# Kernel tuning notes

Measured on AMD Instinct MI355X. Metric: run time of the kernel, lower is better.

The kernel has to match this reference:

```python
import jax, jax.numpy as jnp
import numpy as np

C, H, W = 64, 32, 32
N = 32
HW = H * W
EPS = 1e-5


def setup_inputs() -> dict:
    kk = jax.random.key(0)
    ks = jax.random.split(kk, 6)
    shp = (N, C, H, W)
    return {
        "query": jax.random.normal(ks[0], shp, jnp.float32),
        "key": jax.random.normal(ks[1], shp, jnp.float32),
        "value": jax.random.normal(ks[2], shp, jnp.float32),
        "ln1_w": jnp.ones((C, H, W), jnp.float32),
        "ln1_b": jnp.zeros((C, H, W), jnp.float32),
        "ln2_w": jnp.ones((C, H, W), jnp.float32),
        "ln2_b": jnp.zeros((C, H, W), jnp.float32),
        "ln3_w": jnp.ones((C, H, W), jnp.float32),
        "ln3_b": jnp.zeros((C, H, W), jnp.float32),
        "wq": jax.random.normal(ks[3], (C, C), jnp.float32) / np.sqrt(C).astype(np.float32),
        "bq": jnp.zeros((C,), jnp.float32),
        "wk": jax.random.normal(ks[4], (C, C), jnp.float32) / np.sqrt(C).astype(np.float32),
        "bk": jnp.zeros((C,), jnp.float32),
        "wv": jax.random.normal(ks[5], (C, C), jnp.float32) / np.sqrt(C).astype(np.float32),
        "bv": jnp.zeros((C,), jnp.float32),
    }


def _ln(x, w, b):
    # LayerNorm over the full (C,H,W) normalized_shape, as nn.LayerNorm(dim)
    mu = jnp.mean(x, axis=(1, 2, 3), keepdims=True)
    var = jnp.var(x, axis=(1, 2, 3), keepdims=True)
    return (x - mu) * jax.lax.rsqrt(var + EPS) * w + b


def _proj(x, w, b):
    # 1x1 conv == per-pixel channel mixing; output reshaped to (N, C, H*W)
    y = jnp.einsum('oc,nchw->nohw', w, x) + b[None, :, None, None]
    return y.reshape(x.shape[0], C, HW)


def reference(query, key, value, ln1_w, ln1_b, ln2_w, ln2_b, ln3_w, ln3_b,
              wq, bq, wk, bk, wv, bv):
    qn = _ln(query, ln1_w, ln1_b)
    kn = _ln(key, ln2_w, ln2_b)
    vn = _ln(value, ln3_w, ln3_b)
    q = _proj(qn, wq, bq)   # (N, C, HW)
    k = _proj(kn, wk, bk)
    v = _proj(vn, wv, bv)
    # attention[n,i,j] = sum_c k[n,c,i] * q[n,c,j] / sqrt(C); softmax over dim=1 (i)
    attn = jnp.einsum('nci,ncj->nij', k, q) / jnp.sqrt(jnp.float32(C))
    attn = jax.nn.softmax(attn, axis=1)
    # output = v @ attn : (N, C, HW)
    out = jnp.einsum('nci,nij->ncj', v, attn).reshape(qn.shape)
    # residual adds the NORMALIZED query (that's what SelfAttention receives)
    x = (qn + out).reshape(qn.shape[0], -1)  # (N, C*H*W)
    return x, attn
```

## Files before the change

kernel.cpp:

```cpp
#include <hip/hip_runtime.h>
#include <math.h>

#define NB   32
#define CCH  64
#define HWD  1024
#define CHW  65536
#define EPSV 1e-5f

typedef __attribute__((ext_vector_type(8))) short bf16x8;
typedef __attribute__((ext_vector_type(4))) float f32x4;

__device__ __forceinline__ unsigned f2b(float x) {
    union { float f; unsigned u; } v; v.f = x;
    return (v.u + 0x7fffu + ((v.u >> 16) & 1u)) >> 16;
}
__device__ __forceinline__ float b2f(unsigned short u) {
    union { unsigned u; float f; } v; v.u = ((unsigned)u) << 16;
    return v.f;
}

__global__ __launch_bounds__(256)
void k_stats(const float* __restrict__ q, const float* __restrict__ k,
             const float* __restrict__ v, float* __restrict__ part)
{
    const int chunk = blockIdx.x, which = blockIdx.y, n = blockIdx.z;
    const float* x = (which == 0) ? q : (which == 1 ? k : v);
    const float4* x4 = (const float4*)(x + (size_t)n * CHW) + chunk * 2048;
    float s = 0.f, ss = 0.f;
#pragma unroll
    for (int i = 0; i < 8; ++i) {
        float4 t = x4[threadIdx.x + i * 256];
        s  += t.x + t.y + t.z + t.w;
        ss += t.x * t.x + t.y * t.y + t.z * t.z + t.w * t.w;
    }
    __shared__ float rs[256], rss[256];
    rs[threadIdx.x] = s; rss[threadIdx.x] = ss;
    __syncthreads();
    for (int off = 128; off > 0; off >>= 1) {
        if (threadIdx.x < off) {
            rs[threadIdx.x]  += rs[threadIdx.x + off];
            rss[threadIdx.x] += rss[threadIdx.x + off];
        }
        __syncthreads();
    }
    if (threadIdx.x == 0) {
        const int b = (n * 3 + which) * 8 + chunk;
        part[b * 2 + 0] = rs[0];
        part[b * 2 + 1] = rss[0];
    }
}

__global__ __launch_bounds__(256, 4)
void k_proj(const float* __restrict__ q,  const float* __restrict__ k,  const float* __restrict__ v,
            const float* __restrict__ w1, const float* __restrict__ b1,
            const float* __restrict__ w2, const float* __restrict__ b2,
            const float* __restrict__ w3, const float* __restrict__ b3,
            const float* __restrict__ wq, const float* __restrict__ bq,
            const float* __restrict__ wk, const float* __restrict__ bk,
            const float* __restrict__ wv, const float* __restrict__ bv,
            const float* __restrict__ part,
            float* __restrict__ qn, short* __restrict__ pqt,
            short* __restrict__ pkt, short* __restrict__ pvb)
{
    __shared__ float xn[64][68];
    __shared__ float wt[64][68];
    __shared__ float musd[6];
    const int pt = blockIdx.x, n = blockIdx.y;
    const int t = threadIdx.x;

    if (t < 3) {
        float s = 0.f, ss = 0.f;
#pragma unroll
        for (int cidx = 0; cidx < 8; ++cidx) {
            const int b = (n * 3 + t) * 8 + cidx;
            s  += part[b * 2 + 0];
            ss += part[b * 2 + 1];
        }
        const float mu = s * (1.0f / CHW);
        musd[t * 2 + 0] = mu;
        musd[t * 2 + 1] = rsqrtf(ss * (1.0f / CHW) - mu * mu + EPSV);
    }
    __syncthreads();

    const float* src[3]   = {q, k, v};
    const float* lw[3]    = {w1, w2, w3};
    const float* lb[3]    = {b1, b2, b3};
    const float* pw[3]    = {wq, wk, wv};
    const float* pbias[3] = {bq, bk, bv};
    const int p   = t & 63;
    const int ob  = (t >> 6) * 16;
    const int pix = pt * 64 + p;

    for (int tt = 0; tt < 3; ++tt) {
        for (int idx = t; idx < 4096; idx += 256) {
            const int o = idx >> 6, c = idx & 63;
            wt[c][o] = pw[tt][idx];
        }
        const float mu = musd[tt * 2], is = musd[tt * 2 + 1];
        for (int idx = t; idx < 1024; idx += 256) {
            const int c = idx >> 4, p4 = idx & 15;
            const int gi = c * HWD + pt * 64 + p4 * 4;
            float4 xv = *(const float4*)&src[tt][(size_t)n * CHW + gi];
            float4 w4 = *(const float4*)&lw[tt][gi];
            float4 b4 = *(const float4*)&lb[tt][gi];
            float4 r;
            r.x = (xv.x - mu) * is * w4.x + b4.x;
            r.y = (xv.y - mu) * is * w4.y + b4.y;
            r.z = (xv.z - mu) * is * w4.z + b4.z;
            r.w = (xv.w - mu) * is * w4.w + b4.w;
            *(float4*)&xn[c][p4 * 4] = r;
            if (tt == 0) *(float4*)&qn[(size_t)n * CHW + gi] = r;
        }
        __syncthreads();

        float acc[16];
#pragma unroll
        for (int i = 0; i < 16; ++i) acc[i] = pbias[tt][ob + i];
#pragma unroll 4
        for (int c = 0; c < 64; ++c) {
            const float xv = xn[c][p];
#pragma unroll
            for (int o4 = 0; o4 < 4; ++o4) {
                float4 w4 = *(const float4*)&wt[c][ob + o4 * 4];
                acc[o4 * 4 + 0] += w4.x * xv;
                acc[o4 * 4 + 1] += w4.y * xv;
                acc[o4 * 4 + 2] += w4.z * xv;
                acc[o4 * 4 + 3] += w4.w * xv;
            }
        }
        if (tt == 2) {
#pragma unroll
            for (int i = 0; i < 16; ++i)
                pvb[(size_t)n * CHW + (ob + i) * HWD + pix] = (short)f2b(acc[i]);
        } else {
            const float sc = (tt == 0) ? 0.125f : 1.0f;
            unsigned u[8];
#pragma unroll
            for (int i = 0; i < 8; ++i)
                u[i] = (f2b(acc[2 * i + 1] * sc) << 16) | f2b(acc[2 * i] * sc);
            short* dst = (tt == 0) ? pqt : pkt;
            *(uint4*)&dst[(size_t)n * CHW + pix * 64 + ob]     = *(uint4*)&u[0];
            *(uint4*)&dst[(size_t)n * CHW + pix * 64 + ob + 8] = *(uint4*)&u[4];
        }
        __syncthreads();
    }
}

__global__ __launch_bounds__(512, 4)
void k_attn3(const short* __restrict__ pqt, const short* __restrict__ pkt,
             const short* __restrict__ pvb, const float* __restrict__ qn,
             float* __restrict__ xout, float* __restrict__ attn)
{
    __shared__ __align__(16) char smem[65536 + 4608 + 2048];
    short* q_lds = (short*)(smem + 65536);
    float* wredM = (float*)(smem + 65536 + 4608);
    float* wredS = wredM + 256;

    const int wg  = blockIdx.x;
    const int xcd = wg & 7, lid = wg >> 3;
    const int n   = xcd * 4 + (lid >> 5);
    const int jb  = lid & 31;
    const size_t nb = (size_t)n * CHW;
    const int t = threadIdx.x;
    const int w = t >> 6;
    const int l = t & 63;
    const int l15 = l & 15, lg = l >> 4;
    const int ibase = w * 128;

    if (t < 256) {
        const int j = t >> 3, c8 = (t & 7) * 8;
        *(bf16x8*)&q_lds[j * 72 + c8] =
            *(const bf16x8*)&pqt[nb + (size_t)(jb * 32 + j) * 64 + c8];
    }
    __syncthreads();

    f32x4 acc[8][2] = {};
#pragma unroll
    for (int ks = 0; ks < 2; ++ks) {
        bf16x8 bqf[2];
#pragma unroll
        for (int jt = 0; jt < 2; ++jt)
            bqf[jt] = *(const bf16x8*)&q_lds[(jt * 16 + l15) * 72 + ks * 32 + lg * 8];
#pragma unroll
        for (int f = 0; f < 8; ++f) {
            const int i = ibase + f * 16 + l15;
            bf16x8 af = *(const bf16x8*)&pkt[nb + (size_t)i * 64 + ks * 32 + lg * 8];
#pragma unroll
            for (int jt = 0; jt < 2; ++jt)
                acc[f][jt] = __builtin_amdgcn_mfma_f32_16x16x32_bf16(
                    af, bqf[jt], acc[f][jt], 0, 0, 0);
        }
    }

    float mself[2];
#pragma unroll
    for (int jt = 0; jt < 2; ++jt) {
        float m = -1e30f;
#pragma unroll
        for (int f = 0; f < 8; ++f)
#pragma unroll
            for (int r = 0; r < 4; ++r) m = fmaxf(m, acc[f][jt][r]);
        m = fmaxf(m, __shfl_xor(m, 16));
        m = fmaxf(m, __shfl_xor(m, 32));
        mself[jt] = m;
        float s = 0.f;
#pragma unroll
        for (int f = 0; f < 8; ++f)
#pragma unroll
            for (int r = 0; r < 4; ++r) {
                float e = __expf(acc[f][jt][r] - m);
                acc[f][jt][r] = e;
                s += e;
            }
        s += __shfl_xor(s, 16);
        s += __shfl_xor(s, 32);
        if (l < 16) {
            wredM[w * 32 + jt * 16 + l] = m;
            wredS[w * 32 + jt * 16 + l] = s;
        }
    }
    __syncthreads();

#pragma unroll
    for (int jt = 0; jt < 2; ++jt) {
        const int j = jt * 16 + l15;
        float M = wredM[j];
#pragma unroll
        for (int ww = 1; ww < 8; ++ww) M = fmaxf(M, wredM[ww * 32 + j]);
        float S = 0.f;
#pragma unroll
        for (int ww = 0; ww < 8; ++ww)
            S += wredS[ww * 32 + j] * __expf(wredM[ww * 32 + j] - M);
        const float fac = __expf(mself[jt] - M) / S;
#pragma unroll
        for (int f = 0; f < 8; ++f) {
            const int i0 = ibase + f * 16 + lg * 4;
            uint2 pw;
            pw.x = (f2b(acc[f][jt][1] * fac) << 16) | f2b(acc[f][jt][0] * fac);
            pw.y = (f2b(acc[f][jt][3] * fac) << 16) | f2b(acc[f][jt][2] * fac);
            const unsigned byte = (unsigned)j * 2048u + (((unsigned)i0 * 2u) ^ (((unsigned)j & 7u) << 4));
            *(uint2*)(smem + byte) = pw;
        }
    }
    __syncthreads();

    if (w < 4) {
        f32x4 oacc[2] = {};
        __builtin_amdgcn_s_setprio(1);
#pragma unroll 4
        for (int ks = 0; ks < 32; ++ks) {
            bf16x8 av = *(const bf16x8*)&pvb[nb + (size_t)(w * 16 + l15) * HWD + ks * 32 + lg * 8];
            const unsigned ib = (unsigned)(ks * 32 + lg * 8) * 2u;
#pragma unroll
            for (int u = 0; u < 2; ++u) {
                const int j = u * 16 + l15;
                bf16x8 bp = *(const bf16x8*)(smem + (unsigned)j * 2048u + (ib ^ (((unsigned)j & 7u) << 4)));
                oacc[u] = __builtin_amdgcn_mfma_f32_16x16x32_bf16(av, bp, oacc[u], 0, 0, 0);
            }
        }
        __builtin_amdgcn_s_setprio(0);
#pragma unroll
        for (int u = 0; u < 2; ++u) {
            const int j = u * 16 + l15;
#pragma unroll
            for (int r = 0; r < 4; ++r) {
                const int c = w * 16 + lg * 4 + r;
                const size_t o = nb + (size_t)c * HWD + jb * 32 + j;
                xout[o] = oacc[u][r] + qn[o];
            }
        }
    } else {
        float* aout = attn + (size_t)n * HWD * HWD + jb * 32;
        const int jq   = (l & 7) * 4;
        const int isub = l >> 3;
        const int i00  = (w - 4) * 256;
#pragma unroll 4
        for (int g = 0; g < 32; ++g) {
            const int i = i00 + g * 8 + isub;
            f32x4 o4;
#pragma unroll
            for (int r = 0; r < 4; ++r) {
                const unsigned j = (unsigned)(jq + r);
                const unsigned byte = j * 2048u + (((unsigned)i * 2u) ^ ((j & 7u) << 4));
                o4[r] = b2f(*(const unsigned short*)(smem + byte));
            }
            __builtin_nontemporal_store(o4, (f32x4*)&aout[(size_t)i * HWD + jq]);
        }
    }
}

extern "C" void kernel_launch(void* const* d_in, const int* in_sizes, int n_in,
                              void* d_out, int out_size, void* d_ws, size_t ws_size,
                              hipStream_t stream)
{
    const float* q  = (const float*)d_in[0];
    const float* k  = (const float*)d_in[1];
    const float* v  = (const float*)d_in[2];
    const float* w1 = (const float*)d_in[3];
    const float* b1 = (const float*)d_in[4];
    const float* w2 = (const float*)d_in[5];
    const float* b2 = (const float*)d_in[6];
    const float* w3 = (const float*)d_in[7];
    const float* b3 = (const float*)d_in[8];
    const float* wq = (const float*)d_in[9];
    const float* bq = (const float*)d_in[10];
    const float* wk = (const float*)d_in[11];
    const float* bk = (const float*)d_in[12];
    const float* wv = (const float*)d_in[13];
    const float* bv = (const float*)d_in[14];

    float* ws   = (float*)d_ws;
    float* part = ws;
    float* qn   = ws + 4096;
    short* pqt  = (short*)(qn + 2097152);
    short* pkt  = pqt + 2097152;
    short* pvb  = pkt + 2097152;

    float* xout = (float*)d_out;
    float* attn = xout + 2097152;

    k_stats<<<dim3(8, 3, 32), 256, 0, stream>>>(q, k, v, part);
    k_proj<<<dim3(16, 32), 256, 0, stream>>>(q, k, v, w1, b1, w2, b2, w3, b3,
                                             wq, bq, wk, bk, wv, bv,
                                             part, qn, pqt, pkt, pvb);
    k_attn3<<<dim3(1024), dim3(512), 0, stream>>>(pqt, pkt, pvb, qn, xout, attn);
}
```

Measured before the change: 89.13 us.

## Compute QKV projections with bf16 MFMA using hi/lo split weights

Replaces the fp32 scalar FMA loop of the 1x1-conv projections with bf16 MFMA 16x16x32 instructions. Weights are loaded straight from global into registers and split into bf16 hi and lo parts to keep precision, while the normalized activations are staged in LDS as transposed bf16. This drops the fp32 weight-transpose tile in shared memory and its stores. It costs extra conversion work and bf16 rounding of the activations, which changes numerics slightly.

```diff
diff --git a/kernel.cpp b/kernel.cpp
--- a/kernel.cpp
+++ b/kernel.cpp
@@ -62,11 +62,12 @@
             float* __restrict__ qn, short* __restrict__ pqt,
             short* __restrict__ pkt, short* __restrict__ pvb)
 {
-    __shared__ float xn[64][68];
-    __shared__ float wt[64][68];
+    __shared__ short xnb[64][72];
     __shared__ float musd[6];
     const int pt = blockIdx.x, n = blockIdx.y;
     const int t = threadIdx.x;
+    const int w = t >> 6, l = t & 63;
+    const int l15 = l & 15, lg = l >> 4;
 
     if (t < 3) {
         float s = 0.f, ss = 0.f;
@@ -87,15 +88,25 @@
     const float* lb[3]    = {b1, b2, b3};
     const float* pw[3]    = {wq, wk, wv};
     const float* pbias[3] = {bq, bk, bv};
-    const int p   = t & 63;
-    const int ob  = (t >> 6) * 16;
-    const int pix = pt * 64 + p;
 
     for (int tt = 0; tt < 3; ++tt) {
-        for (int idx = t; idx < 4096; idx += 256) {
-            const int o = idx >> 6, c = idx & 63;
-            wt[c][o] = pw[tt][idx];
-        }
+        const float sc = (tt == 0) ? 0.125f : 1.0f;
+
+        bf16x8 whi[2], wlo[2];
+#pragma unroll
+        for (int ks = 0; ks < 2; ++ks) {
+            float wf[8];
+            *(float4*)&wf[0] = *(const float4*)&pw[tt][(w * 16 + l15) * 64 + ks * 32 + lg * 8];
+            *(float4*)&wf[4] = *(const float4*)&pw[tt][(w * 16 + l15) * 64 + ks * 32 + lg * 8 + 4];
+#pragma unroll
+            for (int e = 0; e < 8; ++e) {
+                const float ws = wf[e] * sc;
+                const unsigned hi = f2b(ws);
+                whi[ks][e] = (short)hi;
+                wlo[ks][e] = (short)f2b(ws - b2f((unsigned short)hi));
+            }
+        }
+
         const float mu = musd[tt * 2], is = musd[tt * 2 + 1];
         for (int idx = t; idx < 1024; idx += 256) {
             const int c = idx >> 4, p4 = idx & 15;
@@ -108,39 +119,50 @@
             r.y = (xv.y - mu) * is * w4.y + b4.y;
             r.z = (xv.z - mu) * is * w4.z + b4.z;
             r.w = (xv.w - mu) * is * w4.w + b4.w;
-            *(float4*)&xn[c][p4 * 4] = r;
             if (tt == 0) *(float4*)&qn[(size_t)n * CHW + gi] = r;
+            xnb[p4 * 4 + 0][c] = (short)f2b(r.x);
+            xnb[p4 * 4 + 1][c] = (short)f2b(r.y);
+            xnb[p4 * 4 + 2][c] = (short)f2b(r.z);
+            xnb[p4 * 4 + 3][c] = (short)f2b(r.w);
         }
         __syncthreads();
 
-        float acc[16];
-#pragma unroll
-        for (int i = 0; i < 16; ++i) acc[i] = pbias[tt][ob + i];
-#pragma unroll 4
-        for (int c = 0; c < 64; ++c) {
-            const float xv = xn[c][p];
-#pragma unroll
-            for (int o4 = 0; o4 < 4; ++o4) {
-                float4 w4 = *(const float4*)&wt[c][ob + o4 * 4];
-                acc[o4 * 4 + 0] += w4.x * xv;
-                acc[o4 * 4 + 1] += w4.y * xv;
-                acc[o4 * 4 + 2] += w4.z * xv;
-                acc[o4 * 4 + 3] += w4.w * xv;
-            }
-        }
-        if (tt == 2) {
-#pragma unroll
-            for (int i = 0; i < 16; ++i)
-                pvb[(size_t)n * CHW + (ob + i) * HWD + pix] = (short)f2b(acc[i]);
+        if (tt < 2) {
+            const float4 bb = *(const float4*)&pbias[tt][w * 16 + lg * 4];
+            short* dst = (tt == 0) ? pqt : pkt;
+#pragma unroll
+            for (int pt4 = 0; pt4 < 4; ++pt4) {
+                f32x4 acc = {};
+#pragma unroll
+                for (int ks = 0; ks < 2; ++ks) {
+                    bf16x8 xb = *(const bf16x8*)&xnb[pt4 * 16 + l15][ks * 32 + lg * 8];
+                    acc = __builtin_amdgcn_mfma_f32_16x16x32_bf16(whi[ks], xb, acc, 0, 0, 0);
+                    acc = __builtin_amdgcn_mfma_f32_16x16x32_bf16(wlo[ks], xb, acc, 0, 0, 0);
+                }
+                const int pix = pt * 64 + pt4 * 16 + l15;
+                uint2 u;
+                u.x = (f2b(acc[1] + bb.y * sc) << 16) | f2b(acc[0] + bb.x * sc);
+                u.y = (f2b(acc[3] + bb.w * sc) << 16) | f2b(acc[2] + bb.z * sc);
+                *(uint2*)&dst[(size_t)n * CHW + pix * 64 + w * 16 + lg * 4] = u;
+            }
         } else {
-            const float sc = (tt == 0) ? 0.125f : 1.0f;
-            unsigned u[8];
-#pragma unroll
-            for (int i = 0; i < 8; ++i)
-                u[i] = (f2b(acc[2 * i + 1] * sc) << 16) | f2b(acc[2 * i] * sc);
-            short* dst = (tt == 0) ? pqt : pkt;
-            *(uint4*)&dst[(size_t)n * CHW + pix * 64 + ob]     = *(uint4*)&u[0];
-            *(uint4*)&dst[(size_t)n * CHW + pix * 64 + ob + 8] = *(uint4*)&u[4];
+            const float bo = pbias[2][w * 16 + l15];
+#pragma unroll
+            for (int pt4 = 0; pt4 < 4; ++pt4) {
+                f32x4 acc = {};
+#pragma unroll
+                for (int ks = 0; ks < 2; ++ks) {
+                    bf16x8 xb = *(const bf16x8*)&xnb[pt4 * 16 + l15][ks * 32 + lg * 8];
+                    acc = __builtin_amdgcn_mfma_f32_16x16x32_bf16(xb, whi[ks], acc, 0, 0, 0);
+                    acc = __builtin_amdgcn_mfma_f32_16x16x32_bf16(xb, wlo[ks], acc, 0, 0, 0);
+                }
+                const int o   = w * 16 + l15;
+                const int px4 = pt * 64 + pt4 * 16 + lg * 4;
+                uint2 u;
+                u.x = (f2b(acc[1] + bo) << 16) | f2b(acc[0] + bo);
+                u.y = (f2b(acc[3] + bo) << 16) | f2b(acc[2] + bo);
+                *(uint2*)&pvb[(size_t)n * CHW + o * HWD + px4] = u;
+            }
         }
         __syncthreads();
     }
```

Measured after the change: 74.03 us. -16.9%, faster.
